# Optimization experiments

Measured on AMD Instinct MI355X. Metric: run time of the kernel, lower is better.

The kernel has to match this reference:

```python
import jax, jax.numpy as jnp
import numpy as np

N_HEADS = 16

def _rope(x):
    # x: (B, T, H, D); rotary embedding over sequence positions T
    B, T, H, D = x.shape
    half = D // 2
    freqs = 1.0 / (10000.0 ** (jnp.arange(half, dtype=x.dtype) / half))
    t = jnp.arange(T, dtype=x.dtype)
    ang = t[:, None] * freqs[None, :]            # (T, half)
    cos = jnp.cos(ang)[:, None, :]               # (T, 1, half) broadcast over heads
    sin = jnp.sin(ang)[:, None, :]
    x1, x2 = x[..., :half], x[..., half:]
    return jnp.concatenate([x1 * cos - x2 * sin, x1 * sin + x2 * cos], axis=-1)


def setup_inputs() -> dict:
    key = jax.random.key(0)
    kx, kq, kk, kv, ko = jax.random.split(key, 5)
    B, T, C = 4, 2048, 2048
    x = jax.random.normal(kx, (B, T, C), dtype=jnp.float32)
    # TPLinear (tp_size=1): weight (out_f, in_f), init randn*0.02, no bias
    wq = jax.random.normal(kq, (C, C), dtype=jnp.float32) * 0.02
    wk = jax.random.normal(kk, (C, C), dtype=jnp.float32) * 0.02
    wv = jax.random.normal(kv, (C, C), dtype=jnp.float32) * 0.02
    wo = jax.random.normal(ko, (C, C), dtype=jnp.float32) * 0.02
    return {"x": x, "wq": wq, "wk": wk, "wv": wv, "wo": wo}


def reference(x, wq, wk, wv, wo):
    B, T, C = x.shape
    H = N_HEADS
    D = C // H
    # QKV projections (F.linear: x @ W^T)
    q = (x @ wq.T).reshape(B, T, H, D)
    k = (x @ wk.T).reshape(B, T, H, D)
    v = (x @ wv.T).reshape(B, T, H, D)
    # RoPE on q and k over sequence positions
    q = _rope(q).transpose(0, 2, 1, 3)           # (B, H, T, D)
    k = _rope(k).transpose(0, 2, 1, 3)
    v = v.transpose(0, 2, 1, 3)
    # Causal scaled dot-product attention
    scale = 1.0 / jnp.sqrt(jnp.asarray(D, dtype=x.dtype))
    scores = jnp.einsum("bhqd,bhkd->bhqk", q, k) * scale   # (B, H, T, T)
    causal = jnp.tril(jnp.ones((T, T), dtype=bool))
    scores = jnp.where(causal, scores, jnp.finfo(x.dtype).min)
    att = jax.nn.softmax(scores, axis=-1)
    out = jnp.einsum("bhqk,bhkd->bhqd", att, v)            # (B, H, T, D)
    out = out.transpose(0, 2, 1, 3).reshape(B, T, C)
    return out @ wo.T
```

## Files before the change

kernel.cpp:

```cpp
#include <hip/hip_runtime.h>
#include <hip/hip_bf16.h>
#include <stdint.h>

typedef __hip_bfloat16 bf16;
typedef __bf16 bf16x8_t __attribute__((ext_vector_type(8)));
typedef float f32x4_t __attribute__((ext_vector_type(4)));

#define GAS __attribute__((address_space(1)))
#define LAS __attribute__((address_space(3)))
#define SCHED0 __builtin_amdgcn_sched_barrier(0)

__device__ __forceinline__ f32x4_t mfma16(bf16x8_t a, bf16x8_t b, f32x4_t c) {
    return __builtin_amdgcn_mfma_f32_16x16x32_bf16(a, b, c, 0, 0, 0);
}

__device__ __forceinline__ void gload_lds16(const void* g, void* l) {
    __builtin_amdgcn_global_load_lds((const GAS void*)g, (LAS void*)l, 16, 0, 0);
}

__device__ __forceinline__ float exp2_fast(float x) {
    float r;
    asm volatile("v_exp_f32 %0, %1\n\ts_nop 0" : "=v"(r) : "v"(x));
    return r;
}

__global__ __launch_bounds__(256) void cast_f32_bf16(const float* __restrict__ in,
                                                     bf16* __restrict__ out, int n4) {
    int stride = gridDim.x * blockDim.x;
    for (int i = blockIdx.x * blockDim.x + threadIdx.x; i < n4; i += stride) {
        float4 f = reinterpret_cast<const float4*>(in)[i];
        bf16 h0 = __float2bfloat16(f.x), h1 = __float2bfloat16(f.y);
        bf16 h2 = __float2bfloat16(f.z), h3 = __float2bfloat16(f.w);
        ushort4 u;
        u.x = *reinterpret_cast<unsigned short*>(&h0);
        u.y = *reinterpret_cast<unsigned short*>(&h1);
        u.z = *reinterpret_cast<unsigned short*>(&h2);
        u.w = *reinterpret_cast<unsigned short*>(&h3);
        reinterpret_cast<ushort4*>(out)[i] = u;
    }
}

__device__ __forceinline__ void store_out(float* p, float v) { *p = v; }
__device__ __forceinline__ void store_out(bf16* p, float v) { *p = __float2bfloat16(v); }

#define BAR()   do { SCHED0; __builtin_amdgcn_s_barrier(); SCHED0; } while (0)
#define LGKM0() do { asm volatile("s_waitcnt lgkmcnt(0)" ::: "memory"); SCHED0; } while (0)
#define VM4()   do { asm volatile("s_waitcnt vmcnt(4)" ::: "memory"); SCHED0; } while (0)

#define READ_A(P, MLO)                                                          \
    do {                                                                        \
        const char* la_ = lds + (P) * 65536;                                    \
        _Pragma("unroll") for (int kk = 0; kk < 2; ++kk)                        \
        _Pragma("unroll") for (int f = 0; f < 4; ++f) {                         \
            int r_ = wm * 128 + ((MLO) + f) * 16 + li;                          \
            af[kk][(MLO) + f] = *reinterpret_cast<const bf16x8_t*>(             \
                la_ + r_ * 128 + ((kk * 64 + hi * 16) ^ (l7 << 4)));            \
        }                                                                       \
    } while (0)

#define READ_B(P, NLO)                                                          \
    do {                                                                        \
        const char* lb_ = lds + (P) * 65536 + 32768;                            \
        _Pragma("unroll") for (int kk = 0; kk < 2; ++kk)                        \
        _Pragma("unroll") for (int g = 0; g < 2; ++g) {                         \
            int r_ = wn * 64 + ((NLO) + g) * 16 + li;                           \
            bfr[kk][(NLO) + g] = *reinterpret_cast<const bf16x8_t*>(            \
                lb_ + r_ * 128 + ((kk * 64 + hi * 16) ^ (l7 << 4)));            \
        }                                                                       \
    } while (0)

#define MFMA_Q(MLO, NLO)                                                        \
    do {                                                                        \
        __builtin_amdgcn_s_setprio(1);                                          \
        _Pragma("unroll") for (int kk = 0; kk < 2; ++kk)                        \
        _Pragma("unroll") for (int f = 0; f < 4; ++f)                           \
        _Pragma("unroll") for (int g = 0; g < 2; ++g)                           \
            acc[(MLO) + f][(NLO) + g] = mfma16(af[kk][(MLO) + f],               \
                                               bfr[kk][(NLO) + g],              \
                                               acc[(MLO) + f][(NLO) + g]);      \
        __builtin_amdgcn_s_setprio(0);                                          \
    } while (0)

template <typename OutT>
__global__ __launch_bounds__(512, 2) void gemm_nt256(const bf16* __restrict__ A,
                                                     const bf16* __restrict__ B,
                                                     OutT* __restrict__ C,
                                                     int M, int N, int K) {
    __shared__ char lds[131072];
    const int t = threadIdx.x, lane = t & 63, w = t >> 6;
    const int wm = w >> 2, wn = w & 3;
    const int li = lane & 15, hi = lane >> 4, l7 = lane & 7, l3 = lane >> 3;

    const int ny = M >> 8;
    const int cpx = gridDim.x >> 3;
    const int tile = ((int)blockIdx.x & 7) * cpx + ((int)blockIdx.x >> 3);
    const int m0 = (tile % ny) * 256, n0 = (tile / ny) * 256;
    const int NT = K >> 6;

    f32x4_t acc[8][4];
#pragma unroll
    for (int f = 0; f < 8; ++f)
#pragma unroll
        for (int g = 0; g < 4; ++g) acc[f][g] = f32x4_t{0.f, 0.f, 0.f, 0.f};

    bf16x8_t af[2][8], bfr[2][4];

    auto stage_half = [&](int kt, int half, int p) {
        kt = kt < NT - 1 ? kt : NT - 1;
        const bf16* src = (half >= 2) ? B : A;
        const int rb = ((half >= 2) ? n0 : m0) + (half & 1) * 128;
        char* dst = lds + p * 65536 + (half >= 2 ? 32768 : 0) + (half & 1) * 16384;
        const int sc = (l7 ^ l3) << 4;
#pragma unroll
        for (int l = 0; l < 2; ++l) {
            int row = rb + l * 64 + w * 8 + l3;
            gload_lds16((const char*)src + (size_t)row * K * 2 + (size_t)kt * 128 + sc,
                        dst + (l * 64 + w * 8) * 128);
        }
    };

    stage_half(0, 0, 0); stage_half(0, 1, 0); stage_half(0, 2, 0); stage_half(0, 3, 0);
    stage_half(1, 0, 1); stage_half(1, 1, 1);
    VM4(); BAR();

    const int NITER = NT >> 1;
    for (int j = 0; j < NITER; ++j) {
        const int t1 = 2 * j + 1;
        READ_A(0, 0); READ_B(0, 0); stage_half(t1, 2, 1);
        BAR(); LGKM0(); MFMA_Q(0, 0); BAR();
        READ_A(0, 4); READ_B(0, 2); stage_half(t1, 3, 1);
        BAR(); LGKM0(); MFMA_Q(0, 2); BAR();
        stage_half(t1 + 1, 0, 0);
        BAR(); MFMA_Q(4, 0); BAR();
        stage_half(t1 + 1, 1, 0);
        BAR(); MFMA_Q(4, 2); VM4(); BAR();
        READ_A(1, 0); READ_B(1, 0); stage_half(t1 + 1, 2, 0);
        BAR(); LGKM0(); MFMA_Q(0, 0); BAR();
        READ_A(1, 4); READ_B(1, 2); stage_half(t1 + 1, 3, 0);
        BAR(); LGKM0(); MFMA_Q(0, 2); BAR();
        stage_half(t1 + 2, 0, 1);
        BAR(); MFMA_Q(4, 0); BAR();
        stage_half(t1 + 2, 1, 1);
        BAR(); MFMA_Q(4, 2); VM4(); BAR();
    }

#pragma unroll
    for (int f = 0; f < 8; ++f)
#pragma unroll
        for (int g = 0; g < 4; ++g)
#pragma unroll
            for (int r = 0; r < 4; ++r) {
                int row = m0 + wm * 128 + f * 16 + hi * 4 + r;
                int col = n0 + wn * 64 + g * 16 + li;
                store_out(C + (size_t)row * N + col, acc[f][g][r]);
            }
}

__global__ __launch_bounds__(256) void rope_qk(bf16* __restrict__ q, bf16* __restrict__ k,
                                               int total) {
    int idx = blockIdx.x * blockDim.x + threadIdx.x;
    if (idx >= total) return;
    int d = idx & 63;
    int h = (idx >> 6) & 15;
    int bt = idx >> 10;
    int tpos = bt & 2047;
    float freq = expf(-0.14391157f * (float)d);
    float ang = (float)tpos * freq;
    float s, c;
    sincosf(ang, &s, &c);
    size_t base = (size_t)bt * 2048 + h * 128 + d;
    const float scale_q = 0.12751682f;
    {
        float x1 = __bfloat162float(q[base]);
        float x2 = __bfloat162float(q[base + 64]);
        q[base]      = __float2bfloat16((x1 * c - x2 * s) * scale_q);
        q[base + 64] = __float2bfloat16((x1 * s + x2 * c) * scale_q);
    }
    {
        float x1 = __bfloat162float(k[base]);
        float x2 = __bfloat162float(k[base + 64]);
        k[base]      = __float2bfloat16(x1 * c - x2 * s);
        k[base + 64] = __float2bfloat16(x1 * s + x2 * c);
    }
}

__global__ __launch_bounds__(256) void transpose_v(const bf16* __restrict__ v,
                                                   bf16* __restrict__ vT) {
    __shared__ bf16 tile[64][65];
    const int T = 2048, Cc = 2048;
    int bh = blockIdx.z, b = bh >> 4, h = bh & 15;
    int t0 = blockIdx.x * 64, d0 = blockIdx.y * 64;
    int tx = threadIdx.x & 63, ty = threadIdx.x >> 6;
#pragma unroll
    for (int i = 0; i < 16; i++) {
        int tt = ty + i * 4;
        tile[tt][tx] = v[(size_t)(b * T + t0 + tt) * Cc + h * 128 + d0 + tx];
    }
    __syncthreads();
#pragma unroll
    for (int i = 0; i < 16; i++) {
        int dd = ty + i * 4;
        vT[(size_t)(bh * 128 + d0 + dd) * T + t0 + tx] = tile[tx][dd];
    }
}

__global__ __launch_bounds__(256) void flash_attn(const bf16* __restrict__ q,
                                                  const bf16* __restrict__ k,
                                                  const bf16* __restrict__ vT,
                                                  bf16* __restrict__ att) {
    const int T = 2048, Cc = 2048;
    __shared__ bf16 Ks[64 * 128];
    __shared__ bf16 VTs[128 * 64];
    __shared__ bf16 Ps[4][16 * 72];
    const int t = threadIdx.x, lane = t & 63, w = t >> 6;
    const int bh = blockIdx.y, b = bh >> 4, h = bh & 15;
    const int col = lane & 15, hi = lane >> 4;

    for (int pass = 0; pass < 2; ++pass) {
        const int qblk = pass ? (31 - (int)blockIdx.x) : (int)blockIdx.x;
        const int q0 = qblk * 64;

        bf16x8_t qf[4];
        {
            int qrow = q0 + w * 16 + col;
            const char* qb = (const char*)q + ((size_t)(b * T + qrow) * Cc + h * 128) * 2;
#pragma unroll
            for (int kf = 0; kf < 4; kf++)
                qf[kf] = *reinterpret_cast<const bf16x8_t*>(qb + kf * 64 + hi * 16);
        }

        f32x4_t acc[8];
#pragma unroll
        for (int i = 0; i < 8; i++) acc[i] = f32x4_t{0.f, 0.f, 0.f, 0.f};
        float m_run[4] = {-1e30f, -1e30f, -1e30f, -1e30f};
        float l_run[4] = {0.f, 0.f, 0.f, 0.f};

        const int ntiles = qblk + 1;
        for (int ti = 0; ti < ntiles; ++ti) {
            const int k0 = ti * 64;
#pragma unroll
            for (int i = 0; i < 4; ++i) {
                int o = (i * 256 + t) * 16;
                int kr = o >> 8, kc = (o & 255) ^ ((kr & 7) << 4);
                gload_lds16((const char*)k + ((size_t)(b * T + k0 + kr) * Cc + h * 128) * 2 + kc,
                            (char*)Ks + (i * 256 + w * 64) * 16);
                int vr = o >> 7, vc = (o & 127) ^ ((vr & 7) << 4);
                gload_lds16((const char*)vT + ((size_t)(bh * 128 + vr) * T + k0) * 2 + vc,
                            (char*)VTs + (i * 256 + w * 64) * 16);
            }
            __syncthreads();

            f32x4_t s[4];
#pragma unroll
            for (int nb = 0; nb < 4; nb++) {
                s[nb] = f32x4_t{0.f, 0.f, 0.f, 0.f};
#pragma unroll
                for (int kf = 0; kf < 4; kf++) {
                    bf16x8_t kfr = *reinterpret_cast<const bf16x8_t*>(
                        (const char*)Ks + (((nb * 16 + col) * 256 + kf * 64 + hi * 16)
                                           ^ ((col & 7) << 4)));
                    s[nb] = mfma16(qf[kf], kfr, s[nb]);
                }
            }

            const int rowb = q0 + w * 16 + (hi << 2);
            float mt[4] = {-1e30f, -1e30f, -1e30f, -1e30f};
#pragma unroll
            for (int nb = 0; nb < 4; nb++) {
                int kc = k0 + nb * 16 + col;
#pragma unroll
                for (int r = 0; r < 4; r++) {
                    float v = s[nb][r];
                    if (kc > rowb + r) v = -1e30f;
                    s[nb][r] = v;
                    mt[r] = fmaxf(mt[r], v);
                }
            }
#pragma unroll
            for (int r = 0; r < 4; r++) {
#pragma unroll
                for (int mk = 1; mk < 16; mk <<= 1)
                    mt[r] = fmaxf(mt[r], __shfl_xor(mt[r], mk, 64));
            }
            float alpha[4], ls[4];
#pragma unroll
            for (int r = 0; r < 4; r++) {
                float mn = fmaxf(m_run[r], mt[r]);
                alpha[r] = exp2_fast(m_run[r] - mn);
                m_run[r] = mn;
                ls[r] = 0.f;
            }
#pragma unroll
            for (int nb = 0; nb < 4; nb++)
#pragma unroll
                for (int r = 0; r < 4; r++) {
                    float p = exp2_fast(s[nb][r] - m_run[r]);
                    s[nb][r] = p;
                    ls[r] += p;
                }
#pragma unroll
            for (int r = 0; r < 4; r++) {
#pragma unroll
                for (int mk = 1; mk < 16; mk <<= 1)
                    ls[r] += __shfl_xor(ls[r], mk, 64);
                l_run[r] = l_run[r] * alpha[r] + ls[r];
            }
#pragma unroll
            for (int i = 0; i < 8; i++)
#pragma unroll
                for (int r = 0; r < 4; r++) acc[i][r] *= alpha[r];

#pragma unroll
            for (int nb = 0; nb < 4; nb++)
#pragma unroll
                for (int r = 0; r < 4; r++)
                    Ps[w][((hi << 2) + r) * 72 + nb * 16 + col] =
                        __float2bfloat16(s[nb][r]);
            asm volatile("s_waitcnt lgkmcnt(0)" ::: "memory");
            __builtin_amdgcn_sched_barrier(0);
            bf16x8_t pf[2];
#pragma unroll
            for (int kb = 0; kb < 2; kb++)
                pf[kb] = *reinterpret_cast<const bf16x8_t*>(
                    (const char*)Ps[w] + col * 144 + kb * 64 + hi * 16);

#pragma unroll
            for (int db = 0; db < 8; db++)
#pragma unroll
                for (int kb = 0; kb < 2; kb++) {
                    bf16x8_t vf = *reinterpret_cast<const bf16x8_t*>(
                        (const char*)VTs + (((db * 16 + col) * 128 + kb * 64 + hi * 16)
                                            ^ ((col & 7) << 4)));
                    acc[db] = mfma16(pf[kb], vf, acc[db]);
                }
            __syncthreads();
        }

#pragma unroll
        for (int r = 0; r < 4; r++) {
            float inv = 1.0f / l_run[r];
            int row = q0 + w * 16 + (hi << 2) + r;
            size_t base = (size_t)(b * T + row) * Cc + h * 128;
#pragma unroll
            for (int db = 0; db < 8; db++)
                att[base + db * 16 + col] = __float2bfloat16(acc[db][r] * inv);
        }
    }
}

extern "C" void kernel_launch(void* const* d_in, const int* in_sizes, int n_in,
                              void* d_out, int out_size, void* d_ws, size_t ws_size,
                              hipStream_t stream) {
    const int B = 4, T = 2048, C = 2048;
    const int M = B * T;
    const float* x  = (const float*)d_in[0];
    const float* wq = (const float*)d_in[1];
    const float* wk = (const float*)d_in[2];
    const float* wv = (const float*)d_in[3];
    const float* wo = (const float*)d_in[4];
    float* out = (float*)d_out;

    char* ws = (char*)d_ws;
    const size_t SZ_X = (size_t)M * C * 2;
    const size_t SZ_W = (size_t)C * C * 2;
    bf16* xb   = (bf16*)(ws);
    bf16* wqb  = (bf16*)(ws + SZ_X);
    bf16* wkb  = (bf16*)(ws + SZ_X + SZ_W);
    bf16* wvb  = (bf16*)(ws + SZ_X + 2 * SZ_W);
    bf16* wob  = (bf16*)(ws + SZ_X + 3 * SZ_W);
    bf16* qb   = (bf16*)(ws + SZ_X + 4 * SZ_W);
    bf16* kb   = (bf16*)(ws + 2 * SZ_X + 4 * SZ_W);
    bf16* vb   = (bf16*)(ws + 3 * SZ_X + 4 * SZ_W);
    bf16* vTb  = (bf16*)(ws + 4 * SZ_X + 4 * SZ_W);
    bf16* attb = (bf16*)(ws + 5 * SZ_X + 4 * SZ_W);

    cast_f32_bf16<<<2048, 256, 0, stream>>>(x, xb, M * C / 4);
    cast_f32_bf16<<<1024, 256, 0, stream>>>(wq, wqb, C * C / 4);
    cast_f32_bf16<<<1024, 256, 0, stream>>>(wk, wkb, C * C / 4);
    cast_f32_bf16<<<1024, 256, 0, stream>>>(wv, wvb, C * C / 4);
    cast_f32_bf16<<<1024, 256, 0, stream>>>(wo, wob, C * C / 4);

    const int nblk = (M / 256) * (C / 256);
    gemm_nt256<bf16><<<nblk, 512, 0, stream>>>(xb, wqb, qb, M, C, C);
    gemm_nt256<bf16><<<nblk, 512, 0, stream>>>(xb, wkb, kb, M, C, C);
    gemm_nt256<bf16><<<nblk, 512, 0, stream>>>(xb, wvb, vb, M, C, C);

    int rope_total = B * T * 16 * 64;
    rope_qk<<<rope_total / 256, 256, 0, stream>>>(qb, kb, rope_total);

    transpose_v<<<dim3(T / 64, 2, B * 16), 256, 0, stream>>>(vb, vTb);

    flash_attn<<<dim3(16, B * 16), 256, 0, stream>>>(qb, kb, vTb, attb);

    gemm_nt256<float><<<nblk, 512, 0, stream>>>(attb, wob, out, M, C, C);
}
```

Before: 712.6 us.

## Streamline flash attention softmax, merge weight casts, cheapen RoPE trig

```diff
diff --git a/kernel.cpp b/kernel.cpp
--- a/kernel.cpp
+++ b/kernel.cpp
@@ -21,6 +21,16 @@
 __device__ __forceinline__ float exp2_fast(float x) {
     float r;
     asm volatile("v_exp_f32 %0, %1\n\ts_nop 0" : "=v"(r) : "v"(x));
+    return r;
+}
+__device__ __forceinline__ float sin2pi(float x) {
+    float r;
+    asm volatile("v_sin_f32 %0, %1\n\ts_nop 0" : "=v"(r) : "v"(x));
+    return r;
+}
+__device__ __forceinline__ float cos2pi(float x) {
+    float r;
+    asm volatile("v_cos_f32 %0, %1\n\ts_nop 0" : "=v"(r) : "v"(x));
     return r;
 }
 
@@ -29,6 +39,29 @@
     int stride = gridDim.x * blockDim.x;
     for (int i = blockIdx.x * blockDim.x + threadIdx.x; i < n4; i += stride) {
         float4 f = reinterpret_cast<const float4*>(in)[i];
+        bf16 h0 = __float2bfloat16(f.x), h1 = __float2bfloat16(f.y);
+        bf16 h2 = __float2bfloat16(f.z), h3 = __float2bfloat16(f.w);
+        ushort4 u;
+        u.x = *reinterpret_cast<unsigned short*>(&h0);
+        u.y = *reinterpret_cast<unsigned short*>(&h1);
+        u.z = *reinterpret_cast<unsigned short*>(&h2);
+        u.w = *reinterpret_cast<unsigned short*>(&h3);
+        reinterpret_cast<ushort4*>(out)[i] = u;
+    }
+}
+
+__global__ __launch_bounds__(256) void cast_w4(const float* __restrict__ w0,
+                                               const float* __restrict__ w1,
+                                               const float* __restrict__ w2,
+                                               const float* __restrict__ w3,
+                                               bf16* __restrict__ out) {
+    const int n4each = 1 << 20;
+    int stride = gridDim.x * blockDim.x;
+    for (int i = blockIdx.x * blockDim.x + threadIdx.x; i < 4 * n4each; i += stride) {
+        int li = i & (n4each - 1);
+        const float* src = (i < 2 * n4each) ? (i < n4each ? w0 : w1)
+                                            : (i < 3 * n4each ? w2 : w3);
+        float4 f = reinterpret_cast<const float4*>(src)[li];
         bf16 h0 = __float2bfloat16(f.x), h1 = __float2bfloat16(f.y);
         bf16 h2 = __float2bfloat16(f.z), h3 = __float2bfloat16(f.w);
         ushort4 u;
@@ -156,31 +189,32 @@
             }
 }
 
-__global__ __launch_bounds__(256) void rope_qk(bf16* __restrict__ q, bf16* __restrict__ k,
-                                               int total) {
+__global__ __launch_bounds__(256) void rope_qk(bf16* __restrict__ q, bf16* __restrict__ k) {
     int idx = blockIdx.x * blockDim.x + threadIdx.x;
-    if (idx >= total) return;
     int d = idx & 63;
-    int h = (idx >> 6) & 15;
-    int bt = idx >> 10;
+    int bt = idx >> 6;
     int tpos = bt & 2047;
-    float freq = expf(-0.14391157f * (float)d);
-    float ang = (float)tpos * freq;
-    float s, c;
-    sincosf(ang, &s, &c);
-    size_t base = (size_t)bt * 2048 + h * 128 + d;
+    float frev = exp2_fast((float)d * -0.20762051f) * 0.15915494f;
+    float rev = (float)tpos * frev;
+    rev -= floorf(rev);
+    float s = sin2pi(rev), c = cos2pi(rev);
     const float scale_q = 0.12751682f;
-    {
-        float x1 = __bfloat162float(q[base]);
-        float x2 = __bfloat162float(q[base + 64]);
-        q[base]      = __float2bfloat16((x1 * c - x2 * s) * scale_q);
-        q[base + 64] = __float2bfloat16((x1 * s + x2 * c) * scale_q);
-    }
-    {
-        float x1 = __bfloat162float(k[base]);
-        float x2 = __bfloat162float(k[base + 64]);
-        k[base]      = __float2bfloat16(x1 * c - x2 * s);
-        k[base + 64] = __float2bfloat16(x1 * s + x2 * c);
+    size_t base0 = (size_t)bt * 2048 + d;
+#pragma unroll 4
+    for (int h = 0; h < 16; ++h) {
+        size_t base = base0 + h * 128;
+        {
+            float x1 = __bfloat162float(q[base]);
+            float x2 = __bfloat162float(q[base + 64]);
+            q[base]      = __float2bfloat16((x1 * c - x2 * s) * scale_q);
+            q[base + 64] = __float2bfloat16((x1 * s + x2 * c) * scale_q);
+        }
+        {
+            float x1 = __bfloat162float(k[base]);
+            float x2 = __bfloat162float(k[base + 64]);
+            k[base]      = __float2bfloat16(x1 * c - x2 * s);
+            k[base + 64] = __float2bfloat16(x1 * s + x2 * c);
+        }
     }
 }
 
@@ -233,7 +267,7 @@
 #pragma unroll
         for (int i = 0; i < 8; i++) acc[i] = f32x4_t{0.f, 0.f, 0.f, 0.f};
         float m_run[4] = {-1e30f, -1e30f, -1e30f, -1e30f};
-        float l_run[4] = {0.f, 0.f, 0.f, 0.f};
+        float lp[4] = {0.f, 0.f, 0.f, 0.f};
 
         const int ntiles = qblk + 1;
         for (int ti = 0; ti < ntiles; ++ti) {
@@ -251,6 +285,7 @@
             __syncthreads();
 
             f32x4_t s[4];
+            __builtin_amdgcn_s_setprio(1);
 #pragma unroll
             for (int nb = 0; nb < 4; nb++) {
                 s[nb] = f32x4_t{0.f, 0.f, 0.f, 0.f};
@@ -262,19 +297,27 @@
                     s[nb] = mfma16(qf[kf], kfr, s[nb]);
                 }
             }
+            __builtin_amdgcn_s_setprio(0);
 
             const int rowb = q0 + w * 16 + (hi << 2);
             float mt[4] = {-1e30f, -1e30f, -1e30f, -1e30f};
-#pragma unroll
-            for (int nb = 0; nb < 4; nb++) {
-                int kc = k0 + nb * 16 + col;
-#pragma unroll
-                for (int r = 0; r < 4; r++) {
-                    float v = s[nb][r];
-                    if (kc > rowb + r) v = -1e30f;
-                    s[nb][r] = v;
-                    mt[r] = fmaxf(mt[r], v);
+            if (ti == qblk) {
+#pragma unroll
+                for (int nb = 0; nb < 4; nb++) {
+                    int kc = k0 + nb * 16 + col;
+#pragma unroll
+                    for (int r = 0; r < 4; r++) {
+                        float v = s[nb][r];
+                        if (kc > rowb + r) v = -1e30f;
+                        s[nb][r] = v;
+                        mt[r] = fmaxf(mt[r], v);
+                    }
                 }
+            } else {
+#pragma unroll
+                for (int nb = 0; nb < 4; nb++)
+#pragma unroll
+                    for (int r = 0; r < 4; r++) mt[r] = fmaxf(mt[r], s[nb][r]);
             }
 #pragma unroll
             for (int r = 0; r < 4; r++) {
@@ -282,33 +325,33 @@
                 for (int mk = 1; mk < 16; mk <<= 1)
                     mt[r] = fmaxf(mt[r], __shfl_xor(mt[r], mk, 64));
             }
-            float alpha[4], ls[4];
-#pragma unroll
-            for (int r = 0; r < 4; r++) {
-                float mn = fmaxf(m_run[r], mt[r]);
-                alpha[r] = exp2_fast(m_run[r] - mn);
-                m_run[r] = mn;
-                ls[r] = 0.f;
-            }
+
+            float need = -1e30f;
+#pragma unroll
+            for (int r = 0; r < 4; r++) need = fmaxf(need, mt[r] - m_run[r]);
+            if (__any(need > 8.f)) {
+                float alpha[4];
+#pragma unroll
+                for (int r = 0; r < 4; r++) {
+                    float mn = fmaxf(m_run[r], mt[r]);
+                    alpha[r] = exp2_fast(m_run[r] - mn);
+                    m_run[r] = mn;
+                    lp[r] *= alpha[r];
+                }
+#pragma unroll
+                for (int i = 0; i < 8; i++)
+#pragma unroll
+                    for (int r = 0; r < 4; r++) acc[i][r] *= alpha[r];
+            }
+
 #pragma unroll
             for (int nb = 0; nb < 4; nb++)
 #pragma unroll
                 for (int r = 0; r < 4; r++) {
                     float p = exp2_fast(s[nb][r] - m_run[r]);
                     s[nb][r] = p;
-                    ls[r] += p;
+                    lp[r] += p;
                 }
-#pragma unroll
-            for (int r = 0; r < 4; r++) {
-#pragma unroll
-                for (int mk = 1; mk < 16; mk <<= 1)
-                    ls[r] += __shfl_xor(ls[r], mk, 64);
-                l_run[r] = l_run[r] * alpha[r] + ls[r];
-            }
-#pragma unroll
-            for (int i = 0; i < 8; i++)
-#pragma unroll
-                for (int r = 0; r < 4; r++) acc[i][r] *= alpha[r];
 
 #pragma unroll
             for (int nb = 0; nb < 4; nb++)
@@ -324,6 +367,7 @@
                 pf[kb] = *reinterpret_cast<const bf16x8_t*>(
                     (const char*)Ps[w] + col * 144 + kb * 64 + hi * 16);
 
+            __builtin_amdgcn_s_setprio(1);
 #pragma unroll
             for (int db = 0; db < 8; db++)
 #pragma unroll
@@ -333,12 +377,19 @@
                                             ^ ((col & 7) << 4)));
                     acc[db] = mfma16(pf[kb], vf, acc[db]);
                 }
+            __builtin_amdgcn_s_setprio(0);
             __syncthreads();
         }
 
 #pragma unroll
         for (int r = 0; r < 4; r++) {
-            float inv = 1.0f / l_run[r];
+#pragma unroll
+            for (int mk = 1; mk < 16; mk <<= 1)
+                lp[r] += __shfl_xor(lp[r], mk, 64);
+        }
+#pragma unroll
+        for (int r = 0; r < 4; r++) {
+            float inv = 1.0f / lp[r];
             int row = q0 + w * 16 + (hi << 2) + r;
             size_t base = (size_t)(b * T + row) * Cc + h * 128;
 #pragma unroll
@@ -365,28 +416,24 @@
     const size_t SZ_W = (size_t)C * C * 2;
     bf16* xb   = (bf16*)(ws);
     bf16* wqb  = (bf16*)(ws + SZ_X);
-    bf16* wkb  = (bf16*)(ws + SZ_X + SZ_W);
-    bf16* wvb  = (bf16*)(ws + SZ_X + 2 * SZ_W);
-    bf16* wob  = (bf16*)(ws + SZ_X + 3 * SZ_W);
     bf16* qb   = (bf16*)(ws + SZ_X + 4 * SZ_W);
     bf16* kb   = (bf16*)(ws + 2 * SZ_X + 4 * SZ_W);
     bf16* vb   = (bf16*)(ws + 3 * SZ_X + 4 * SZ_W);
     bf16* vTb  = (bf16*)(ws + 4 * SZ_X + 4 * SZ_W);
     bf16* attb = (bf16*)(ws + 5 * SZ_X + 4 * SZ_W);
+    bf16* wkb = wqb + (size_t)C * C;
+    bf16* wvb = wkb + (size_t)C * C;
+    bf16* wob = wvb + (size_t)C * C;
 
     cast_f32_bf16<<<2048, 256, 0, stream>>>(x, xb, M * C / 4);
-    cast_f32_bf16<<<1024, 256, 0, stream>>>(wq, wqb, C * C / 4);
-    cast_f32_bf16<<<1024, 256, 0, stream>>>(wk, wkb, C * C / 4);
-    cast_f32_bf16<<<1024, 256, 0, stream>>>(wv, wvb, C * C / 4);
-    cast_f32_bf16<<<1024, 256, 0, stream>>>(wo, wob, C * C / 4);
+    cast_w4<<<2048, 256, 0, stream>>>(wq, wk, wv, wo, wqb);
 
     const int nblk = (M / 256) * (C / 256);
     gemm_nt256<bf16><<<nblk, 512, 0, stream>>>(xb, wqb, qb, M, C, C);
     gemm_nt256<bf16><<<nblk, 512, 0, stream>>>(xb, wkb, kb, M, C, C);
     gemm_nt256<bf16><<<nblk, 512, 0, stream>>>(xb, wvb, vb, M, C, C);
 
-    int rope_total = B * T * 16 * 64;
-    rope_qk<<<rope_total / 256, 256, 0, stream>>>(qb, kb, rope_total);
+    rope_qk<<<(B * T * 64) / 256, 256, 0, stream>>>(qb, kb);
 
     transpose_v<<<dim3(T / 64, 2, B * 16), 256, 0, stream>>>(vb, vTb);
 
```

New measurement: 689.4 us. 3.3% less time.
